# Optimization experiments

Hardware: AMD Instinct MI355X
Metric: run time of the kernel (lower is better)

Reference implementation:

```python
import jax, jax.numpy as jnp
import numpy as np

N, E, C, H, DH, NB, NA, FC = 30000, 480000, 128, 8, 16, 32, 16, 64
AH = H * DH  # 128 = attn-heads feature dim = mul_alpha


def smooth_leaky_relu(x, alpha=0.2):
    # Equiformer SmoothLeakyReLU: (1+a)/2 * x + (1-a)/2 * x * (2*sigmoid(x) - 1)
    return 0.5 * (1.0 + alpha) * x + 0.5 * (1.0 - alpha) * x * (2.0 * jax.nn.sigmoid(x) - 1.0)


def setup_inputs() -> dict:
    key = jax.random.key(0)
    ks = jax.random.split(key, 20)

    def rn(k, shape, scale=1.0):
        return jax.random.normal(k, shape, dtype=jnp.float32) * scale

    inp = {
        "node_feats": rn(ks[0], (N, C)),
        "node_attr": rn(ks[1], (N, NA)),
        "edge_attr": rn(ks[2], (E, 1)),          # scalar spherical-harmonic channel
        "edge_embedding": rn(ks[3], (E, NB)),     # radial basis embedding
        # message_src_proj (bias) / message_dst_proj (no bias)
        "W_src": rn(ks[4], (C, C), 1.0 / np.sqrt(C)),
        "b_src": jnp.zeros((C,), jnp.float32),
        "W_dst": rn(ks[5], (C, C), 1.0 / np.sqrt(C)),
        # radial network (dtp_rad) for external TP weights
        "W_fc1": rn(ks[6], (NB + 2 * NA, FC), 1.0 / np.sqrt(NB + 2 * NA)),
        "b_fc1": jnp.zeros((FC,), jnp.float32),
        "W_fc2": rn(ks[7], (FC, FC), 1.0 / np.sqrt(FC)),
        "b_fc2": jnp.zeros((FC,), jnp.float32),
        "W_fc3": rn(ks[8], (FC, C), 1.0 / np.sqrt(FC)),
        # attention_score_net
        "W_alpha": rn(ks[9], (C, AH), 1.0 / np.sqrt(C)),
        # edge_message_net.lin (followed by gate)
        "W_lin": rn(ks[10], (C, C), 1.0 / np.sqrt(C)),
        # value_net internal depthwise-TP weights + its linear
        "w_int": rn(ks[11], (C,)),
        "W_val": rn(ks[12], (C, AH), 1.0 / np.sqrt(C)),
        # attention_dot [num_heads, mul_alpha_head]
        "att_dot": rn(ks[13], (H, DH), 1.0 / np.sqrt(DH)),
        # output projection
        "W_out": rn(ks[14], (AH, C), 1.0 / np.sqrt(AH)),
        "b_out": jnp.zeros((C,), jnp.float32),
        "edge_src": jax.random.randint(ks[15], (E,), 0, N),
        "edge_dst": jax.random.randint(ks[16], (E,), 0, N),
    }
    return inp


def reference(node_feats, node_attr, edge_attr, edge_embedding,
              W_src, b_src, W_dst,
              W_fc1, b_fc1, W_fc2, b_fc2, W_fc3,
              W_alpha, W_lin, w_int, W_val, att_dot, W_out, b_out,
              edge_src, edge_dst):
    # node projections then gather to edges
    msg_src = node_feats @ W_src + b_src
    msg_dst = node_feats @ W_dst
    message = msg_src[edge_src] + msg_dst[edge_dst]                    # [E, C]

    # radial net on concat(edge_embedding, src_attr, dst_attr)
    wf = jnp.concatenate([edge_embedding, node_attr[edge_src], node_attr[edge_dst]], axis=-1)
    h = jax.nn.silu(wf @ W_fc1 + b_fc1)
    h = jax.nn.silu(h @ W_fc2 + b_fc2)
    weight = h @ W_fc3                                                 # [E, C] depthwise-TP weights

    # depthwise tensor product with scalar edge_attr, radial-weighted
    message = message * edge_attr * weight                             # [E, C]

    # attention scores -> heads
    scores = (message @ W_alpha).reshape(E, H, DH)                     # [E, H, DH]

    # value path: lin + gate (SiLU on scalars), internal-weight dtp, lin -> heads
    value = jax.nn.silu(message @ W_lin)                               # [E, C]
    value = value * edge_attr * w_int                                  # [E, C]
    value = (value @ W_val).reshape(E, H, DH)                          # [E, H, DH]

    scores = smooth_leaky_relu(scores)
    logits = jnp.einsum('ehk,hk->eh', scores, att_dot)                 # [E, H]

    # segment softmax over destination nodes (torch_geometric.utils.softmax)
    m = jax.ops.segment_max(logits, edge_dst, num_segments=N)          # [N, H]
    m = jnp.where(jnp.isfinite(m), m, 0.0)
    ex = jnp.exp(logits - m[edge_dst])
    den = jax.ops.segment_sum(ex, edge_dst, num_segments=N)
    alpha = ex / (den[edge_dst] + 1e-16)                               # [E, H]

    # attention-weighted scatter-add aggregation
    out = jax.ops.segment_sum(value * alpha[:, :, None], edge_dst, num_segments=N)  # [N, H, DH]
    out = out.reshape(N, AH)
    return out @ W_out + b_out                                         # [N, C]
```

## Files before the change

kernel.cpp:

```cpp
#include <hip/hip_runtime.h>
#include <hip/hip_bf16.h>
#include <cstdint>
#include <cstddef>


typedef unsigned short u16;
typedef unsigned int u32;
typedef __attribute__((ext_vector_type(8))) short bf16x8;
typedef __attribute__((ext_vector_type(4))) float f32x4;

union fu_ { float f; u32 u; };
static __device__ __forceinline__ float lo2f(u32 v) { fu_ x; x.u = v << 16; return x.f; }
static __device__ __forceinline__ float hi2f(u32 v) { fu_ x; x.u = v & 0xFFFF0000u; return x.f; }
static __device__ __forceinline__ u16 f2bf(float f) {
    union { __hip_bfloat16 h; u16 u; } c;
    c.h = __float2bfloat16(f);
    return c.u;
}
static __device__ __forceinline__ u32 pack2(float a, float b) {
    return (u32)f2bf(a) | ((u32)f2bf(b) << 16);
}
static __device__ __forceinline__ float sigmoidf_(float x) { return 1.0f / (1.0f + __expf(-x)); }
static __device__ __forceinline__ float siluf_(float x)    { return x * sigmoidf_(x); }
static __device__ __forceinline__ float slreluf_(float x)  { return x * (0.2f + 0.8f * sigmoidf_(x)); }

#define MFMA16(a, b, c) __builtin_amdgcn_mfma_f32_16x16x32_bf16((a), (b), (c), 0, 0, 0)

static __device__ __forceinline__ bf16x8 ld8f_bf(const float* __restrict__ p) {
    const float4 x = *reinterpret_cast<const float4*>(p);
    const float4 y = *reinterpret_cast<const float4*>(p + 4);
    bf16x8 r;
    r[0] = (short)f2bf(x.x); r[1] = (short)f2bf(x.y);
    r[2] = (short)f2bf(x.z); r[3] = (short)f2bf(x.w);
    r[4] = (short)f2bf(y.x); r[5] = (short)f2bf(y.y);
    r[6] = (short)f2bf(y.z); r[7] = (short)f2bf(y.w);
    return r;
}

static __device__ __forceinline__ int xcd_swz(int orig, int nwg) {
    const int q = nwg >> 3, rr = nwg & 7;
    const int xcd = orig & 7, idx = orig >> 3;
    return (xcd < rr ? xcd * (q + 1) : rr * (q + 1) + (xcd - rr) * q) + idx;
}

__global__ void hist_k(const int* __restrict__ dst, int* __restrict__ deg, int E) {
    int i = blockIdx.x * blockDim.x + threadIdx.x;
    if (i < E) atomicAdd(&deg[dst[i]], 1);
}

__global__ void scan_k(const int* __restrict__ deg, int* __restrict__ rowptr,
                       int* __restrict__ cursor, int n) {
    __shared__ int part[1024];
    const int t = threadIdx.x;
    const int C = (n + 1023) / 1024;
    const int lo = t * C;
    const int hi = (lo + C < n) ? (lo + C) : n;
    int s = 0;
    for (int i = lo; i < hi; ++i) s += deg[i];
    part[t] = s;
    __syncthreads();
    for (int off = 1; off < 1024; off <<= 1) {
        int v = part[t];
        int u = (t >= off) ? part[t - off] : 0;
        __syncthreads();
        part[t] = v + u;
        __syncthreads();
    }
    int excl = (t == 0) ? 0 : part[t - 1];
    for (int i = lo; i < hi; ++i) {
        rowptr[i] = excl;
        cursor[i] = excl;
        excl += deg[i];
    }
    if (t == 1023) rowptr[n] = part[1023];
}

__global__ void fill_k(const int* __restrict__ dst, int* __restrict__ cursor,
                       int* __restrict__ eids, int E) {
    int i = blockIdx.x * blockDim.x + threadIdx.x;
    if (i < E) {
        int d = dst[i];
        int p = atomicAdd(&cursor[d], 1);
        eids[p] = i;
    }
}

__global__ void prep_w_k(const float* __restrict__ Wa, const float* __restrict__ Wl,
                         const float* __restrict__ Wv,
                         const float* __restrict__ W1, const float* __restrict__ W2,
                         const float* __restrict__ W3,
                         const float* __restrict__ Wsrc, const float* __restrict__ Wdst,
                         const float* __restrict__ Wout,
                         u16* __restrict__ Wct, u16* __restrict__ Wvt,
                         u16* __restrict__ Bt1, u16* __restrict__ Bt2,
                         u16* __restrict__ Bt3,
                         u16* __restrict__ Wst, u16* __restrict__ Wdt,
                         u16* __restrict__ Wot) {
    int idx = blockIdx.x * 256 + threadIdx.x;
    if (idx < 32768) {
        int c = idx >> 7, k = idx & 127;
        float v = (c < 128) ? Wa[(size_t)k * 128 + c] : Wl[(size_t)k * 128 + (c - 128)];
        Wct[idx] = f2bf(v);
    } else if (idx < 49152) {
        int t = idx - 32768;
        int j = t >> 7, c = t & 127;
        Wvt[t] = f2bf(Wv[(size_t)c * 128 + j]);
    } else if (idx < 53248) {
        int t = idx - 49152;
        int c = t >> 6, k = t & 63;
        Bt1[t] = f2bf(W1[(size_t)k * 64 + c]);
    } else if (idx < 57344) {
        int t = idx - 53248;
        int c = t >> 6, k = t & 63;
        Bt2[t] = f2bf(W2[(size_t)k * 64 + c]);
    } else if (idx < 65536) {
        int t = idx - 57344;
        int c = t >> 6, k = t & 63;
        Bt3[t] = f2bf(W3[(size_t)k * 128 + c]);
    } else if (idx < 81920) {
        int t = idx - 65536;
        int c = t >> 7, k = t & 127;
        Wst[t] = f2bf(Wsrc[(size_t)k * 128 + c]);
    } else if (idx < 98304) {
        int t = idx - 81920;
        int c = t >> 7, k = t & 127;
        Wdt[t] = f2bf(Wdst[(size_t)k * 128 + c]);
    } else if (idx < 114688) {
        int t = idx - 98304;
        int c = t >> 7, k = t & 127;
        Wot[t] = f2bf(Wout[(size_t)k * 128 + c]);
    }
}

__global__ __launch_bounds__(256) void proj_mfma_k(const float* __restrict__ A,
                                                   const u16* __restrict__ Wt,
                                                   const float* __restrict__ bias,
                                                   float* __restrict__ Out, int M) {
    const int tid  = threadIdx.x;
    const int lane = tid & 63;
    const int w    = tid >> 6;
    const int lr   = lane & 15;
    const int lg   = lane >> 4;
    const int e0   = blockIdx.x * 64;

    f32x4 acc[4][2];
#pragma unroll
    for (int m = 0; m < 4; ++m)
#pragma unroll
        for (int n = 0; n < 2; ++n) acc[m][n] = (f32x4)(0.0f);

#pragma unroll
    for (int ks = 0; ks < 4; ++ks) {
        const int kk = lg * 8 + ks * 32;
        bf16x8 a[4], b[2];
#pragma unroll
        for (int m = 0; m < 4; ++m) {
            int row = e0 + lr + 16 * m;
            row = (row < M) ? row : (M - 1);
            a[m] = ld8f_bf(&A[(size_t)row * 128 + kk]);
        }
#pragma unroll
        for (int n = 0; n < 2; ++n) {
            const int c = 32 * w + 16 * n + lr;
            b[n] = *reinterpret_cast<const bf16x8*>(&Wt[(size_t)c * 128 + kk]);
        }
#pragma unroll
        for (int m = 0; m < 4; ++m)
#pragma unroll
            for (int n = 0; n < 2; ++n) acc[m][n] = MFMA16(a[m], b[n], acc[m][n]);
    }

#pragma unroll
    for (int n = 0; n < 2; ++n) {
        const int j = 32 * w + 16 * n + lr;
        const float bv = bias ? bias[j] : 0.0f;
#pragma unroll
        for (int m = 0; m < 4; ++m)
#pragma unroll
            for (int i = 0; i < 4; ++i) {
                const int row = e0 + 16 * m + 4 * lg + i;
                if (row < M) Out[(size_t)row * 128 + j] = acc[m][n][i] + bv;
            }
    }
}

__global__ __launch_bounds__(256, 4) void msg_attn_k(
    const float* __restrict__ eemb, const float* __restrict__ nattr,
    const float* __restrict__ ea,
    const int* __restrict__ src, const int* __restrict__ dst,
    const int* __restrict__ eids,
    const u16* __restrict__ Bt1, const float* __restrict__ b1,
    const u16* __restrict__ Bt2, const float* __restrict__ b2,
    const u16* __restrict__ Bt3,
    const float* __restrict__ Ps, const float* __restrict__ Pd,
    const u16* __restrict__ Wct, const u16* __restrict__ Wvt,
    const float* __restrict__ att_dot, const float* __restrict__ w_int,
    float* __restrict__ LG, u16* __restrict__ V, int E) {
    __shared__ __align__(16) char smem[35840];
    char* regA   = smem;
    char* regB   = smem + 16384;
    float* lgs   = (float*)(smem + 32768);
    int*   eid_l = (int*)(smem + 34816);
    int*   src_l = eid_l + 64;
    int*   dst_l = src_l + 64;
    float* ea_l  = (float*)(dst_l + 64);

    const int tid  = threadIdx.x;
    const int lane = tid & 63;
    const int w    = tid >> 6;
    const int lr   = lane & 15;
    const int lg   = lane >> 4;
    const int e0   = xcd_swz(blockIdx.x, gridDim.x) * 64;

    if (tid < 64) {
        int slot = e0 + tid;
        int e = (slot < E) ? eids[slot] : eids[E - 1];
        eid_l[tid] = e;
        src_l[tid] = src[e];
        dst_l[tid] = dst[e];
        ea_l[tid]  = ea[e];
    }
    __syncthreads();

    {
        f32x4 acc1[4];
#pragma unroll
        for (int m = 0; m < 4; ++m) acc1[m] = (f32x4)(0.0f);
#pragma unroll
        for (int ks = 0; ks < 2; ++ks) {
            const int kk = lg * 8 + ks * 32;
            bf16x8 a[4];
#pragma unroll
            for (int m = 0; m < 4; ++m) {
                const int r = lr + 16 * m;
                const float* ap;
                if (kk < 32)      ap = &eemb[(size_t)eid_l[r] * 32 + kk];
                else if (kk < 48) ap = &nattr[(size_t)src_l[r] * 16 + (kk - 32)];
                else              ap = &nattr[(size_t)dst_l[r] * 16 + (kk - 48)];
                a[m] = ld8f_bf(ap);
            }
            const bf16x8 b = *reinterpret_cast<const bf16x8*>(&Bt1[(size_t)(16 * w + lr) * 64 + kk]);
#pragma unroll
            for (int m = 0; m < 4; ++m) acc1[m] = MFMA16(a[m], b, acc1[m]);
        }
        const int c = 16 * w + lr;
        const float bias = b1[c];
#pragma unroll
        for (int m = 0; m < 4; ++m)
#pragma unroll
            for (int i = 0; i < 4; ++i) {
                const int r = 16 * m + 4 * lg + i;
                const int byte = (r * 128 + c * 2) ^ ((r & 7) << 4);
                *reinterpret_cast<u16*>(regA + byte) = f2bf(siluf_(acc1[m][i] + bias));
            }
    }
    __syncthreads();

    {
        f32x4 acc2[4];
#pragma unroll
        for (int m = 0; m < 4; ++m) acc2[m] = (f32x4)(0.0f);
#pragma unroll
        for (int ks = 0; ks < 2; ++ks) {
            const int kk = lg * 8 + ks * 32;
            bf16x8 a[4];
#pragma unroll
            for (int m = 0; m < 4; ++m) {
                const int r = lr + 16 * m;
                const int byte = (r * 128 + kk * 2) ^ ((r & 7) << 4);
                a[m] = *reinterpret_cast<const bf16x8*>(regA + byte);
            }
            const bf16x8 b = *reinterpret_cast<const bf16x8*>(&Bt2[(size_t)(16 * w + lr) * 64 + kk]);
#pragma unroll
            for (int m = 0; m < 4; ++m) acc2[m] = MFMA16(a[m], b, acc2[m]);
        }
        const int c = 16 * w + lr;
        const float bias = b2[c];
#pragma unroll
        for (int m = 0; m < 4; ++m)
#pragma unroll
            for (int i = 0; i < 4; ++i) {
                const int r = 16 * m + 4 * lg + i;
                const int byte = (r * 128 + c * 2) ^ ((r & 7) << 4);
                *reinterpret_cast<u16*>(regA + 8192 + byte) = f2bf(siluf_(acc2[m][i] + bias));
            }
    }
    __syncthreads();

    {
        f32x4 acc3[2][4];
#pragma unroll
        for (int n = 0; n < 2; ++n)
#pragma unroll
            for (int m = 0; m < 4; ++m) acc3[n][m] = (f32x4)(0.0f);
#pragma unroll
        for (int ks = 0; ks < 2; ++ks) {
            const int kk = lg * 8 + ks * 32;
            bf16x8 a[4];
#pragma unroll
            for (int m = 0; m < 4; ++m) {
                const int r = lr + 16 * m;
                const int byte = (r * 128 + kk * 2) ^ ((r & 7) << 4);
                a[m] = *reinterpret_cast<const bf16x8*>(regA + 8192 + byte);
            }
            bf16x8 b[2];
#pragma unroll
            for (int n = 0; n < 2; ++n) {
                const int c = 32 * w + 16 * n + lr;
                b[n] = *reinterpret_cast<const bf16x8*>(&Bt3[(size_t)c * 64 + kk]);
            }
#pragma unroll
            for (int n = 0; n < 2; ++n)
#pragma unroll
                for (int m = 0; m < 4; ++m) acc3[n][m] = MFMA16(a[m], b[n], acc3[n][m]);
        }
#pragma unroll
        for (int n = 0; n < 2; ++n) {
            const int c = 32 * w + 16 * n + lr;
#pragma unroll
            for (int m = 0; m < 4; ++m)
#pragma unroll
                for (int i = 0; i < 4; ++i) {
                    const int r = 16 * m + 4 * lg + i;
                    const int byte = (r * 256 + c * 2) ^ ((r & 7) << 4);
                    *reinterpret_cast<u16*>(regB + byte) = f2bf(acc3[n][m][i]);
                }
        }
    }
    __syncthreads();

#pragma unroll
    for (int t = 0; t < 4; ++t) {
        const int idx = tid + 256 * t;
        const int r = idx >> 4;
        const int c8 = (idx & 15) * 8;
        if (e0 + r >= E) continue;
        const int byte = (r * 256 + c8 * 2) ^ ((r & 7) << 4);
        const uint4 wv = *reinterpret_cast<const uint4*>(regB + byte);
        const float wt[8] = {lo2f(wv.x), hi2f(wv.x), lo2f(wv.y), hi2f(wv.y),
                             lo2f(wv.z), hi2f(wv.z), lo2f(wv.w), hi2f(wv.w)};
        const int s = src_l[r], d = dst_l[r];
        const float eav = ea_l[r];
        const float4 ps0 = *reinterpret_cast<const float4*>(&Ps[(size_t)s * 128 + c8]);
        const float4 ps1 = *reinterpret_cast<const float4*>(&Ps[(size_t)s * 128 + c8 + 4]);
        const float4 pd0 = *reinterpret_cast<const float4*>(&Pd[(size_t)d * 128 + c8]);
        const float4 pd1 = *reinterpret_cast<const float4*>(&Pd[(size_t)d * 128 + c8 + 4]);
        float m[8];
        m[0] = (ps0.x + pd0.x) * eav * wt[0];
        m[1] = (ps0.y + pd0.y) * eav * wt[1];
        m[2] = (ps0.z + pd0.z) * eav * wt[2];
        m[3] = (ps0.w + pd0.w) * eav * wt[3];
        m[4] = (ps1.x + pd1.x) * eav * wt[4];
        m[5] = (ps1.y + pd1.y) * eav * wt[5];
        m[6] = (ps1.z + pd1.z) * eav * wt[6];
        m[7] = (ps1.w + pd1.w) * eav * wt[7];
        u32 p0 = pack2(m[0], m[1]), p1 = pack2(m[2], m[3]);
        u32 p2 = pack2(m[4], m[5]), p3 = pack2(m[6], m[7]);
        *reinterpret_cast<uint4*>(regB + byte) = make_uint4(p0, p1, p2, p3);
    }
    __syncthreads();

    const int c0w = w * 64;
#pragma unroll
    for (int n = 0; n < 4; ++n) {
        f32x4 accn[4];
#pragma unroll
        for (int m = 0; m < 4; ++m) accn[m] = (f32x4)(0.0f);
#pragma unroll
        for (int ks = 0; ks < 4; ++ks) {
            const int kk = lg * 8 + ks * 32;
            const bf16x8 b = *reinterpret_cast<const bf16x8*>(
                &Wct[(size_t)(c0w + 16 * n + lr) * 128 + kk]);
#pragma unroll
            for (int m = 0; m < 4; ++m) {
                const int r = lr + 16 * m;
                const int byte = (r * 256 + kk * 2) ^ ((r & 7) << 4);
                const bf16x8 am = *reinterpret_cast<const bf16x8*>(regB + byte);
                accn[m] = MFMA16(am, b, accn[m]);
            }
        }
        if (w < 2) {
            const float ad = att_dot[c0w + 16 * n + lr];
            const int h = 4 * w + n;
#pragma unroll
            for (int m = 0; m < 4; ++m) {
#pragma unroll
                for (int i = 0; i < 4; ++i) {
                    float s = slreluf_(accn[m][i]) * ad;
                    s += __shfl_xor(s, 1);
                    s += __shfl_xor(s, 2);
                    s += __shfl_xor(s, 4);
                    s += __shfl_xor(s, 8);
                    if (lr == 0) lgs[(16 * m + 4 * lg + i) * 8 + h] = s;
                }
            }
        } else {
            const int cc = 64 * (w - 2) + 16 * n + lr;
            const float wi = w_int[cc];
#pragma unroll
            for (int m = 0; m < 4; ++m) {
#pragma unroll
                for (int i = 0; i < 4; ++i) {
                    const int r = 16 * m + 4 * lg + i;
                    const float v1 = siluf_(accn[m][i]) * ea_l[r] * wi;
                    const int byte = (r * 256 + cc * 2) ^ ((r & 7) << 4);
                    *reinterpret_cast<u16*>(regA + byte) = f2bf(v1);
                }
            }
        }
    }
    __syncthreads();

    {
        f32x4 acc2[4][2];
#pragma unroll
        for (int m = 0; m < 4; ++m)
#pragma unroll
            for (int n = 0; n < 2; ++n) acc2[m][n] = (f32x4)(0.0f);
#pragma unroll
        for (int ks = 0; ks < 4; ++ks) {
            const int kk = lg * 8 + ks * 32;
            bf16x8 a2[4], b2[2];
#pragma unroll
            for (int m = 0; m < 4; ++m) {
                const int r = lr + 16 * m;
                const int byte = (r * 256 + kk * 2) ^ ((r & 7) << 4);
                a2[m] = *reinterpret_cast<const bf16x8*>(regA + byte);
            }
#pragma unroll
            for (int n = 0; n < 2; ++n) {
                const int j = 32 * w + 16 * n + lr;
                b2[n] = *reinterpret_cast<const bf16x8*>(&Wvt[(size_t)j * 128 + kk]);
            }
#pragma unroll
            for (int m = 0; m < 4; ++m)
#pragma unroll
                for (int n = 0; n < 2; ++n) acc2[m][n] = MFMA16(a2[m], b2[n], acc2[m][n]);
        }
        u16* Vout = (u16*)regB;
#pragma unroll
        for (int n = 0; n < 2; ++n) {
            const int j = 32 * w + 16 * n + lr;
#pragma unroll
            for (int m = 0; m < 4; ++m)
#pragma unroll
                for (int i = 0; i < 4; ++i) {
                    const int r = 16 * m + 4 * lg + i;
                    Vout[r * 128 + j] = f2bf(acc2[m][n][i]);
                }
        }
    }
    __syncthreads();

    const uint4* vo = reinterpret_cast<const uint4*>(regB);
#pragma unroll
    for (int t = 0; t < 4; ++t) {
        const int idx = tid + 256 * t;
        const int row = idx >> 4;
        if (e0 + row < E)
            *reinterpret_cast<uint4*>(&V[(size_t)e0 * 128 + idx * 8]) = vo[idx];
    }
    if (tid < 128) {
        const int row = tid >> 1;
        if (e0 + row < E)
            *reinterpret_cast<float4*>(&LG[(size_t)e0 * 8 + tid * 4]) =
                *reinterpret_cast<const float4*>(&lgs[tid * 4]);
    }
}

__global__ __launch_bounds__(256) void agg_out_k(const int* __restrict__ rowptr,
                                                 const float* __restrict__ LG,
                                                 const u16* __restrict__ V,
                                                 const u16* __restrict__ Wot,
                                                 const float* __restrict__ b_out,
                                                 float* __restrict__ Out, int Nn) {
    __shared__ __align__(16) char accs[64 * 256];

    const int tid  = threadIdx.x;
    const int lane = tid & 63;
    const int w    = tid >> 6;
    const int lr   = lane & 15;
    const int lg   = lane >> 4;
    const int n0   = xcd_swz(blockIdx.x, gridDim.x) * 64;

    const int h = lane >> 3;
    for (int t = 0; t < 16; ++t) {
        const int node = n0 + 4 * t + w;
        const int r = 4 * t + w;
        if (node < Nn) {
            const int s = rowptr[node], tt = rowptr[node + 1];
            float a0 = 0.0f, a1 = 0.0f, ds = 0.0f;
            int i = s;
            for (; i + 1 < tt; i += 2) {
                const float ex0 = __expf(LG[(size_t)i * 8 + h]);
                const float ex1 = __expf(LG[(size_t)(i + 1) * 8 + h]);
                const u32 v0 = *reinterpret_cast<const u32*>(&V[(size_t)i * 128 + lane * 2]);
                const u32 v1 = *reinterpret_cast<const u32*>(&V[(size_t)(i + 1) * 128 + lane * 2]);
                a0 += ex0 * lo2f(v0) + ex1 * lo2f(v1);
                a1 += ex0 * hi2f(v0) + ex1 * hi2f(v1);
                ds += ex0 + ex1;
            }
            if (i < tt) {
                const float ex0 = __expf(LG[(size_t)i * 8 + h]);
                const u32 v0 = *reinterpret_cast<const u32*>(&V[(size_t)i * 128 + lane * 2]);
                a0 += ex0 * lo2f(v0);
                a1 += ex0 * hi2f(v0);
                ds += ex0;
            }
            const float inv = 1.0f / (ds + 1e-16f);
            const int byte = (r * 256 + lane * 4) ^ ((r & 7) << 4);
            *reinterpret_cast<u32*>(accs + byte) = pack2(a0 * inv, a1 * inv);
        }
    }
    __syncthreads();

    f32x4 acc[4][2];
#pragma unroll
    for (int m = 0; m < 4; ++m)
#pragma unroll
        for (int n = 0; n < 2; ++n) acc[m][n] = (f32x4)(0.0f);

#pragma unroll
    for (int ks = 0; ks < 4; ++ks) {
        const int kk = lg * 8 + ks * 32;
        bf16x8 a[4], b[2];
#pragma unroll
        for (int m = 0; m < 4; ++m) {
            const int r = lr + 16 * m;
            const int byte = (r * 256 + kk * 2) ^ ((r & 7) << 4);
            a[m] = *reinterpret_cast<const bf16x8*>(accs + byte);
        }
#pragma unroll
        for (int n = 0; n < 2; ++n) {
            const int c = 32 * w + 16 * n + lr;
            b[n] = *reinterpret_cast<const bf16x8*>(&Wot[(size_t)c * 128 + kk]);
        }
#pragma unroll
        for (int m = 0; m < 4; ++m)
#pragma unroll
            for (int n = 0; n < 2; ++n) acc[m][n] = MFMA16(a[m], b[n], acc[m][n]);
    }

#pragma unroll
    for (int n = 0; n < 2; ++n) {
        const int j = 32 * w + 16 * n + lr;
        const float bv = b_out[j];
#pragma unroll
        for (int m = 0; m < 4; ++m)
#pragma unroll
            for (int i = 0; i < 4; ++i) {
                const int row = n0 + 16 * m + 4 * lg + i;
                if (row < Nn) Out[(size_t)row * 128 + j] = acc[m][n][i] + bv;
            }
    }
}

extern "C" void kernel_launch(void* const* d_in, const int* in_sizes, int n_in,
                              void* d_out, int out_size, void* d_ws, size_t ws_size,
                              hipStream_t stream) {
    const float* node_feats = (const float*)d_in[0];
    const float* node_attr  = (const float*)d_in[1];
    const float* edge_attr  = (const float*)d_in[2];
    const float* edge_emb   = (const float*)d_in[3];
    const float* W_src      = (const float*)d_in[4];
    const float* b_src      = (const float*)d_in[5];
    const float* W_dst      = (const float*)d_in[6];
    const float* W_fc1      = (const float*)d_in[7];
    const float* b_fc1      = (const float*)d_in[8];
    const float* W_fc2      = (const float*)d_in[9];
    const float* b_fc2      = (const float*)d_in[10];
    const float* W_fc3      = (const float*)d_in[11];
    const float* W_alpha    = (const float*)d_in[12];
    const float* W_lin      = (const float*)d_in[13];
    const float* w_int      = (const float*)d_in[14];
    const float* W_val      = (const float*)d_in[15];
    const float* att_dot    = (const float*)d_in[16];
    const float* W_out      = (const float*)d_in[17];
    const float* b_out      = (const float*)d_in[18];
    const int* esrc         = (const int*)d_in[19];
    const int* edst         = (const int*)d_in[20];

    const int Nn = in_sizes[0] / 128;
    const int E  = in_sizes[19];

    char* w = (char*)d_ws;
    auto alloc = [&](size_t bytes) {
        char* p = w;
        w += (bytes + 255) & ~(size_t)255;
        return p;
    };
    u16* V      = (u16*)alloc((size_t)E * 128 * 2);
    float* LG   = (float*)alloc((size_t)E * 8 * 4);
    float* Psrc = (float*)alloc((size_t)Nn * 128 * 4);
    float* Pdst = (float*)alloc((size_t)Nn * 128 * 4);
    int* deg    = (int*)alloc((size_t)Nn * 4);
    int* rowptr = (int*)alloc((size_t)(Nn + 1) * 4);
    int* cursor = (int*)alloc((size_t)Nn * 4);
    int* eids   = (int*)alloc((size_t)E * 4);
    u16* Wct    = (u16*)alloc(32768 * 2);
    u16* Wvt    = (u16*)alloc(16384 * 2);
    u16* Bt1    = (u16*)alloc(4096 * 2);
    u16* Bt2    = (u16*)alloc(4096 * 2);
    u16* Bt3    = (u16*)alloc(8192 * 2);
    u16* Wst    = (u16*)alloc(16384 * 2);
    u16* Wdt    = (u16*)alloc(16384 * 2);
    u16* Wot    = (u16*)alloc(16384 * 2);

    hipMemsetAsync(deg, 0, (size_t)Nn * 4, stream);
    hist_k<<<(E + 255) / 256, 256, 0, stream>>>(edst, deg, E);
    scan_k<<<1, 1024, 0, stream>>>(deg, rowptr, cursor, Nn);
    fill_k<<<(E + 255) / 256, 256, 0, stream>>>(edst, cursor, eids, E);
    prep_w_k<<<448, 256, 0, stream>>>(W_alpha, W_lin, W_val, W_fc1, W_fc2, W_fc3,
                                      W_src, W_dst, W_out,
                                      Wct, Wvt, Bt1, Bt2, Bt3, Wst, Wdt, Wot);

    const int nb_node = (Nn + 63) / 64;
    const int nb_e    = (E + 63) / 64;

    proj_mfma_k<<<nb_node, 256, 0, stream>>>(node_feats, Wst, b_src, Psrc, Nn);
    proj_mfma_k<<<nb_node, 256, 0, stream>>>(node_feats, Wdt, nullptr, Pdst, Nn);

    msg_attn_k<<<nb_e, 256, 0, stream>>>(edge_emb, node_attr, edge_attr, esrc, edst, eids,
                                         Bt1, b_fc1, Bt2, b_fc2, Bt3,
                                         Psrc, Pdst, Wct, Wvt, att_dot, w_int,
                                         LG, V, E);

    agg_out_k<<<nb_node, 256, 0, stream>>>(rowptr, LG, V, Wot, b_out, (float*)d_out, Nn);
}
```

Before: 498.6 us.

## Fuse src/dst projections with bf16 outputs and split aggregation from output projection

Merges the two node projection kernels into one that reads node_feats once and stores Psrc/Pdst as bf16, halving the bytes gathered per edge in the message kernel. The fused aggregate+outproj kernel is split into a per-node aggregation kernel (one wave per node, 4 nodes per block) writing a bf16 buffer, followed by a separate MFMA output projection. This aims to cut gather bandwidth and improve aggregation parallelism and load balance, at the cost of an extra launch, an extra round trip of the aggregated features through global memory, and bf16 rounding of the projections.

```diff
diff --git a/kernel.cpp b/kernel.cpp
--- a/kernel.cpp
+++ b/kernel.cpp
@@ -132,10 +132,12 @@
     }
 }
 
-__global__ __launch_bounds__(256) void proj_mfma_k(const float* __restrict__ A,
-                                                   const u16* __restrict__ Wt,
-                                                   const float* __restrict__ bias,
-                                                   float* __restrict__ Out, int M) {
+__global__ __launch_bounds__(256) void proj2_mfma_k(const float* __restrict__ A,
+                                                    const u16* __restrict__ Wt1,
+                                                    const u16* __restrict__ Wt2,
+                                                    const float* __restrict__ bias1,
+                                                    u16* __restrict__ O1,
+                                                    u16* __restrict__ O2, int M) {
     const int tid  = threadIdx.x;
     const int lane = tid & 63;
     const int w    = tid >> 6;
@@ -143,16 +145,16 @@
     const int lg   = lane >> 4;
     const int e0   = blockIdx.x * 64;
 
-    f32x4 acc[4][2];
+    f32x4 acc1[4][2], acc2[4][2];
 #pragma unroll
     for (int m = 0; m < 4; ++m)
 #pragma unroll
-        for (int n = 0; n < 2; ++n) acc[m][n] = (f32x4)(0.0f);
+        for (int n = 0; n < 2; ++n) { acc1[m][n] = (f32x4)(0.0f); acc2[m][n] = (f32x4)(0.0f); }
 
 #pragma unroll
     for (int ks = 0; ks < 4; ++ks) {
         const int kk = lg * 8 + ks * 32;
-        bf16x8 a[4], b[2];
+        bf16x8 a[4], b1v[2], b2v[2];
 #pragma unroll
         for (int m = 0; m < 4; ++m) {
             int row = e0 + lr + 16 * m;
@@ -162,24 +164,31 @@
 #pragma unroll
         for (int n = 0; n < 2; ++n) {
             const int c = 32 * w + 16 * n + lr;
-            b[n] = *reinterpret_cast<const bf16x8*>(&Wt[(size_t)c * 128 + kk]);
+            b1v[n] = *reinterpret_cast<const bf16x8*>(&Wt1[(size_t)c * 128 + kk]);
+            b2v[n] = *reinterpret_cast<const bf16x8*>(&Wt2[(size_t)c * 128 + kk]);
         }
 #pragma unroll
         for (int m = 0; m < 4; ++m)
 #pragma unroll
-            for (int n = 0; n < 2; ++n) acc[m][n] = MFMA16(a[m], b[n], acc[m][n]);
+            for (int n = 0; n < 2; ++n) {
+                acc1[m][n] = MFMA16(a[m], b1v[n], acc1[m][n]);
+                acc2[m][n] = MFMA16(a[m], b2v[n], acc2[m][n]);
+            }
     }
 
 #pragma unroll
     for (int n = 0; n < 2; ++n) {
         const int j = 32 * w + 16 * n + lr;
-        const float bv = bias ? bias[j] : 0.0f;
+        const float bv = bias1[j];
 #pragma unroll
         for (int m = 0; m < 4; ++m)
 #pragma unroll
             for (int i = 0; i < 4; ++i) {
                 const int row = e0 + 16 * m + 4 * lg + i;
-                if (row < M) Out[(size_t)row * 128 + j] = acc[m][n][i] + bv;
+                if (row < M) {
+                    O1[(size_t)row * 128 + j] = f2bf(acc1[m][n][i] + bv);
+                    O2[(size_t)row * 128 + j] = f2bf(acc2[m][n][i]);
+                }
             }
     }
 }
@@ -192,7 +201,7 @@
     const u16* __restrict__ Bt1, const float* __restrict__ b1,
     const u16* __restrict__ Bt2, const float* __restrict__ b2,
     const u16* __restrict__ Bt3,
-    const float* __restrict__ Ps, const float* __restrict__ Pd,
+    const u16* __restrict__ Ps, const u16* __restrict__ Pd,
     const u16* __restrict__ Wct, const u16* __restrict__ Wvt,
     const float* __restrict__ att_dot, const float* __restrict__ w_int,
     float* __restrict__ LG, u16* __restrict__ V, int E) {
@@ -341,19 +350,15 @@
                              lo2f(wv.z), hi2f(wv.z), lo2f(wv.w), hi2f(wv.w)};
         const int s = src_l[r], d = dst_l[r];
         const float eav = ea_l[r];
-        const float4 ps0 = *reinterpret_cast<const float4*>(&Ps[(size_t)s * 128 + c8]);
-        const float4 ps1 = *reinterpret_cast<const float4*>(&Ps[(size_t)s * 128 + c8 + 4]);
-        const float4 pd0 = *reinterpret_cast<const float4*>(&Pd[(size_t)d * 128 + c8]);
-        const float4 pd1 = *reinterpret_cast<const float4*>(&Pd[(size_t)d * 128 + c8 + 4]);
+        const uint4 psv = *reinterpret_cast<const uint4*>(&Ps[(size_t)s * 128 + c8]);
+        const uint4 pdv = *reinterpret_cast<const uint4*>(&Pd[(size_t)d * 128 + c8]);
+        const float ps[8] = {lo2f(psv.x), hi2f(psv.x), lo2f(psv.y), hi2f(psv.y),
+                             lo2f(psv.z), hi2f(psv.z), lo2f(psv.w), hi2f(psv.w)};
+        const float pd[8] = {lo2f(pdv.x), hi2f(pdv.x), lo2f(pdv.y), hi2f(pdv.y),
+                             lo2f(pdv.z), hi2f(pdv.z), lo2f(pdv.w), hi2f(pdv.w)};
         float m[8];
-        m[0] = (ps0.x + pd0.x) * eav * wt[0];
-        m[1] = (ps0.y + pd0.y) * eav * wt[1];
-        m[2] = (ps0.z + pd0.z) * eav * wt[2];
-        m[3] = (ps0.w + pd0.w) * eav * wt[3];
-        m[4] = (ps1.x + pd1.x) * eav * wt[4];
-        m[5] = (ps1.y + pd1.y) * eav * wt[5];
-        m[6] = (ps1.z + pd1.z) * eav * wt[6];
-        m[7] = (ps1.w + pd1.w) * eav * wt[7];
+#pragma unroll
+        for (int j = 0; j < 8; ++j) m[j] = (ps[j] + pd[j]) * eav * wt[j];
         u32 p0 = pack2(m[0], m[1]), p1 = pack2(m[2], m[3]);
         u32 p2 = pack2(m[4], m[5]), p3 = pack2(m[6], m[7]);
         *reinterpret_cast<uint4*>(regB + byte) = make_uint4(p0, p1, p2, p3);
@@ -468,51 +473,47 @@
     }
 }
 
-__global__ __launch_bounds__(256) void agg_out_k(const int* __restrict__ rowptr,
-                                                 const float* __restrict__ LG,
-                                                 const u16* __restrict__ V,
-                                                 const u16* __restrict__ Wot,
-                                                 const float* __restrict__ b_out,
-                                                 float* __restrict__ Out, int Nn) {
-    __shared__ __align__(16) char accs[64 * 256];
-
+__global__ __launch_bounds__(256) void aggregate_k(const int* __restrict__ rowptr,
+                                                   const float* __restrict__ LG,
+                                                   const u16* __restrict__ V,
+                                                   u16* __restrict__ ACC, int Nn) {
+    const int node = blockIdx.x * 4 + (threadIdx.x >> 6);
+    const int lane = threadIdx.x & 63;
+    if (node >= Nn) return;
+    const int s = rowptr[node], t = rowptr[node + 1];
+    const int h = lane >> 3;
+    float a0 = 0.0f, a1 = 0.0f, ds = 0.0f;
+    int i = s;
+    for (; i + 1 < t; i += 2) {
+        const float ex0 = __expf(LG[(size_t)i * 8 + h]);
+        const float ex1 = __expf(LG[(size_t)(i + 1) * 8 + h]);
+        const u32 v0 = *reinterpret_cast<const u32*>(&V[(size_t)i * 128 + lane * 2]);
+        const u32 v1 = *reinterpret_cast<const u32*>(&V[(size_t)(i + 1) * 128 + lane * 2]);
+        a0 += ex0 * lo2f(v0) + ex1 * lo2f(v1);
+        a1 += ex0 * hi2f(v0) + ex1 * hi2f(v1);
+        ds += ex0 + ex1;
+    }
+    if (i < t) {
+        const float ex0 = __expf(LG[(size_t)i * 8 + h]);
+        const u32 v0 = *reinterpret_cast<const u32*>(&V[(size_t)i * 128 + lane * 2]);
+        a0 += ex0 * lo2f(v0);
+        a1 += ex0 * hi2f(v0);
+        ds += ex0;
+    }
+    const float inv = 1.0f / (ds + 1e-16f);
+    *reinterpret_cast<u32*>(&ACC[(size_t)node * 128 + lane * 2]) = pack2(a0 * inv, a1 * inv);
+}
+
+__global__ __launch_bounds__(256) void outproj_mfma_k(const u16* __restrict__ A,
+                                                      const u16* __restrict__ Wt,
+                                                      const float* __restrict__ bias,
+                                                      float* __restrict__ Out, int M) {
     const int tid  = threadIdx.x;
     const int lane = tid & 63;
     const int w    = tid >> 6;
     const int lr   = lane & 15;
     const int lg   = lane >> 4;
-    const int n0   = xcd_swz(blockIdx.x, gridDim.x) * 64;
-
-    const int h = lane >> 3;
-    for (int t = 0; t < 16; ++t) {
-        const int node = n0 + 4 * t + w;
-        const int r = 4 * t + w;
-        if (node < Nn) {
-            const int s = rowptr[node], tt = rowptr[node + 1];
-            float a0 = 0.0f, a1 = 0.0f, ds = 0.0f;
-            int i = s;
-            for (; i + 1 < tt; i += 2) {
-                const float ex0 = __expf(LG[(size_t)i * 8 + h]);
-                const float ex1 = __expf(LG[(size_t)(i + 1) * 8 + h]);
-                const u32 v0 = *reinterpret_cast<const u32*>(&V[(size_t)i * 128 + lane * 2]);
-                const u32 v1 = *reinterpret_cast<const u32*>(&V[(size_t)(i + 1) * 128 + lane * 2]);
-                a0 += ex0 * lo2f(v0) + ex1 * lo2f(v1);
-                a1 += ex0 * hi2f(v0) + ex1 * hi2f(v1);
-                ds += ex0 + ex1;
-            }
-            if (i < tt) {
-                const float ex0 = __expf(LG[(size_t)i * 8 + h]);
-                const u32 v0 = *reinterpret_cast<const u32*>(&V[(size_t)i * 128 + lane * 2]);
-                a0 += ex0 * lo2f(v0);
-                a1 += ex0 * hi2f(v0);
-                ds += ex0;
-            }
-            const float inv = 1.0f / (ds + 1e-16f);
-            const int byte = (r * 256 + lane * 4) ^ ((r & 7) << 4);
-            *reinterpret_cast<u32*>(accs + byte) = pack2(a0 * inv, a1 * inv);
-        }
-    }
-    __syncthreads();
+    const int e0   = blockIdx.x * 64;
 
     f32x4 acc[4][2];
 #pragma unroll
@@ -526,14 +527,14 @@
         bf16x8 a[4], b[2];
 #pragma unroll
         for (int m = 0; m < 4; ++m) {
-            const int r = lr + 16 * m;
-            const int byte = (r * 256 + kk * 2) ^ ((r & 7) << 4);
-            a[m] = *reinterpret_cast<const bf16x8*>(accs + byte);
+            int row = e0 + lr + 16 * m;
+            row = (row < M) ? row : (M - 1);
+            a[m] = *reinterpret_cast<const bf16x8*>(&A[(size_t)row * 128 + kk]);
         }
 #pragma unroll
         for (int n = 0; n < 2; ++n) {
             const int c = 32 * w + 16 * n + lr;
-            b[n] = *reinterpret_cast<const bf16x8*>(&Wot[(size_t)c * 128 + kk]);
+            b[n] = *reinterpret_cast<const bf16x8*>(&Wt[(size_t)c * 128 + kk]);
         }
 #pragma unroll
         for (int m = 0; m < 4; ++m)
@@ -544,13 +545,13 @@
 #pragma unroll
     for (int n = 0; n < 2; ++n) {
         const int j = 32 * w + 16 * n + lr;
-        const float bv = b_out[j];
+        const float bv = bias[j];
 #pragma unroll
         for (int m = 0; m < 4; ++m)
 #pragma unroll
             for (int i = 0; i < 4; ++i) {
-                const int row = n0 + 16 * m + 4 * lg + i;
-                if (row < Nn) Out[(size_t)row * 128 + j] = acc[m][n][i] + bv;
+                const int row = e0 + 16 * m + 4 * lg + i;
+                if (row < M) Out[(size_t)row * 128 + j] = acc[m][n][i] + bv;
             }
     }
 }
@@ -591,8 +592,9 @@
     };
     u16* V      = (u16*)alloc((size_t)E * 128 * 2);
     float* LG   = (float*)alloc((size_t)E * 8 * 4);
-    float* Psrc = (float*)alloc((size_t)Nn * 128 * 4);
-    float* Pdst = (float*)alloc((size_t)Nn * 128 * 4);
+    u16* Psrc   = (u16*)alloc((size_t)Nn * 128 * 2);
+    u16* Pdst   = (u16*)alloc((size_t)Nn * 128 * 2);
+    u16* ACC    = (u16*)alloc((size_t)Nn * 128 * 2);
     int* deg    = (int*)alloc((size_t)Nn * 4);
     int* rowptr = (int*)alloc((size_t)(Nn + 1) * 4);
     int* cursor = (int*)alloc((size_t)Nn * 4);
@@ -617,13 +619,14 @@
     const int nb_node = (Nn + 63) / 64;
     const int nb_e    = (E + 63) / 64;
 
-    proj_mfma_k<<<nb_node, 256, 0, stream>>>(node_feats, Wst, b_src, Psrc, Nn);
-    proj_mfma_k<<<nb_node, 256, 0, stream>>>(node_feats, Wdt, nullptr, Pdst, Nn);
+    proj2_mfma_k<<<nb_node, 256, 0, stream>>>(node_feats, Wst, Wdt, b_src, Psrc, Pdst, Nn);
 
     msg_attn_k<<<nb_e, 256, 0, stream>>>(edge_emb, node_attr, edge_attr, esrc, edst, eids,
                                          Bt1, b_fc1, Bt2, b_fc2, Bt3,
                                          Psrc, Pdst, Wct, Wvt, att_dot, w_int,
                                          LG, V, E);
 
-    agg_out_k<<<nb_node, 256, 0, stream>>>(rowptr, LG, V, Wot, b_out, (float*)d_out, Nn);
-}
+    aggregate_k<<<(Nn + 3) / 4, 256, 0, stream>>>(rowptr, LG, V, ACC, Nn);
+
+    outproj_mfma_k<<<nb_node, 256, 0, stream>>>(ACC, Wot, b_out, (float*)d_out, Nn);
+}
```

Measured after the change: 452.0 us. -9.3%, faster.
